# Optimization experiments

Hardware: AMD Instinct MI355X
Metric: run time of the kernel (lower is better)

The kernel has to match this reference:

```python
import jax, jax.numpy as jnp
import numpy as np

TSZ, BSZ, E, H = 1024, 8, 1024, 16


def setup_inputs() -> dict:
    key = jax.random.key(0)
    ks = jax.random.split(key, 7)
    s = 0.02
    return {
        "q": jax.random.normal(ks[0], (TSZ, BSZ, E), jnp.float32),
        "k": jax.random.normal(ks[1], (TSZ, BSZ, E), jnp.float32),
        "v": jax.random.normal(ks[2], (TSZ, BSZ, E), jnp.float32),
        "in_proj_weight": jax.random.normal(ks[3], (3 * E, E), jnp.float32) * s,
        "in_proj_bias": jax.random.normal(ks[4], (3 * E,), jnp.float32) * s,
        "out_proj_weight": jax.random.normal(ks[5], (E, E), jnp.float32) * s,
        "out_proj_bias": jax.random.normal(ks[6], (E,), jnp.float32) * s,
        "num_heads": H,
    }


def reference(q, k, v, in_proj_weight, in_proj_bias, out_proj_weight, out_proj_bias, num_heads):
    tsz, bsz, embed_dim = q.shape
    head_dim = embed_dim // num_heads
    scaling = float(head_dim) ** -0.5

    # in-projections (F.linear: x @ W.T + b), weight sliced into q/k/v chunks
    qp = q @ in_proj_weight[:embed_dim].T + in_proj_bias[:embed_dim]
    kp = k @ in_proj_weight[embed_dim:2 * embed_dim].T + in_proj_bias[embed_dim:2 * embed_dim]
    vp = v @ in_proj_weight[2 * embed_dim:].T + in_proj_bias[2 * embed_dim:]
    qp = qp * scaling

    # (tsz, bsz, E) -> (bsz*H, tsz, head_dim)
    def to_heads(x):
        return x.reshape(tsz, bsz * num_heads, head_dim).transpose(1, 0, 2)

    qh, kh, vh = to_heads(qp), to_heads(kp), to_heads(vp)

    # scaled dot-product attention (no mask, dropout p=0)
    scores = jnp.einsum('bqd,bkd->bqk', qh, kh)  # [bsz*H, tsz, tsz]
    weights = jax.nn.softmax(scores, axis=-1)
    attn = jnp.einsum('bqk,bkd->bqd', weights, vh)

    # back to (tsz, bsz, E), then out projection
    attn = attn.transpose(1, 0, 2).reshape(tsz, bsz, embed_dim)
    out = attn @ out_proj_weight.T + out_proj_bias
    return out
```

## Files before the change

### kernel.cpp

```cpp
#include <hip/hip_runtime.h>

typedef __bf16 bf16;
typedef __attribute__((ext_vector_type(8))) __bf16 v8bf;
typedef __attribute__((ext_vector_type(4))) __bf16 v4bf;
typedef __attribute__((ext_vector_type(4))) float f32x4;

static_assert(sizeof(v8bf) == 16, "v8bf must be 16B");

#define MFMA16(a, b, c) __builtin_amdgcn_mfma_f32_16x16x32_bf16((a), (b), (c), 0, 0, 0)

__device__ __forceinline__ void async_lds16(const bf16* g, bf16* l) {
  __builtin_amdgcn_global_load_lds(
      (__attribute__((address_space(1))) void*)(g),
      (__attribute__((address_space(3))) void*)(l), 16, 0, 0);
}

__global__ __launch_bounds__(256) void cvt_kernel(
    const float* __restrict__ q, const float* __restrict__ k,
    const float* __restrict__ v, const float* __restrict__ wi,
    const float* __restrict__ wo, bf16* __restrict__ xq, bf16* __restrict__ xk,
    bf16* __restrict__ xv, bf16* __restrict__ Wb, bf16* __restrict__ Wob) {
  int idx = blockIdx.x * 256 + threadIdx.x;
  const float4* src;
  v4bf* dst;
  int off;
  if (idx < 2097152)      { src = (const float4*)q;  dst = (v4bf*)xq;  off = idx; }
  else if (idx < 4194304) { src = (const float4*)k;  dst = (v4bf*)xk;  off = idx - 2097152; }
  else if (idx < 6291456) { src = (const float4*)v;  dst = (v4bf*)xv;  off = idx - 4194304; }
  else if (idx < 7077888) { src = (const float4*)wi; dst = (v4bf*)Wb;  off = idx - 6291456; }
  else                    { src = (const float4*)wo; dst = (v4bf*)Wob; off = idx - 7077888; }
  float4 f = src[off];
  v4bf b;
  b[0] = (bf16)f.x; b[1] = (bf16)f.y; b[2] = (bf16)f.z; b[3] = (bf16)f.w;
  dst[off] = b;
}

__global__ __launch_bounds__(256) void qkv_proj_kernel(
    const bf16* __restrict__ xq, const bf16* __restrict__ xk,
    const bf16* __restrict__ xv, const bf16* __restrict__ Wb,
    const float* __restrict__ bias, bf16* __restrict__ oq,
    bf16* __restrict__ ok, bf16* __restrict__ ov) {
  __shared__ bf16 Asm[128 * 64];
  __shared__ bf16 Bsm[128 * 64];
  const int L = blockIdx.x;
  const int rX = L & 7, rest = L >> 3;
  const int m0 = (rX * 8 + (rest & 7)) * 128;
  const int n0 = ((rest >> 3) & 7) * 128;
  const int c = rest >> 6;
  const bf16* X = (c == 0) ? xq : (c == 1) ? xk : xv;
  bf16* outp = (c == 0) ? oq : (c == 1) ? ok : ov;
  const int tid = threadIdx.x;
  const int w = tid >> 6, l = tid & 63, quad = l >> 4, lr = l & 15;
  const int wm = (w & 1) * 64, wn = (w >> 1) * 64;
  const bf16* Wbase = Wb + ((size_t)(c * 1024 + n0)) * 1024;

  int srow[4], skoff[4];
#pragma unroll
  for (int i = 0; i < 4; ++i) {
    const int chunk = i * 256 + tid;
    srow[i] = chunk >> 3;
    skoff[i] = ((chunk & 7) ^ (srow[i] & 7)) * 8;
  }
  int rslot[2];
#pragma unroll
  for (int h = 0; h < 2; ++h) rslot[h] = ((h * 4 + quad) ^ (lr & 7)) * 8;

  f32x4 acc[4][4] = {};
  for (int kt = 0; kt < 16; ++kt) {
    const int k0 = kt * 64;
#pragma unroll
    for (int i = 0; i < 4; ++i) {
      async_lds16(X + (size_t)(m0 + srow[i]) * 1024 + k0 + skoff[i],
                  &Asm[(i * 256 + (tid & ~63)) * 8]);
      async_lds16(Wbase + (size_t)srow[i] * 1024 + k0 + skoff[i],
                  &Bsm[(i * 256 + (tid & ~63)) * 8]);
    }
    __syncthreads();
    v8bf af[4][2], bfm[4][2];
#pragma unroll
    for (int rt = 0; rt < 4; ++rt)
#pragma unroll
      for (int h = 0; h < 2; ++h)
        af[rt][h] = *(const v8bf*)&Asm[(wm + rt * 16 + lr) * 64 + rslot[h]];
#pragma unroll
    for (int ct = 0; ct < 4; ++ct)
#pragma unroll
      for (int h = 0; h < 2; ++h)
        bfm[ct][h] = *(const v8bf*)&Bsm[(wn + ct * 16 + lr) * 64 + rslot[h]];
#pragma unroll
    for (int rt = 0; rt < 4; ++rt)
#pragma unroll
      for (int ct = 0; ct < 4; ++ct) {
        acc[rt][ct] = MFMA16(af[rt][0], bfm[ct][0], acc[rt][ct]);
        acc[rt][ct] = MFMA16(af[rt][1], bfm[ct][1], acc[rt][ct]);
      }
    __syncthreads();
  }

  const float scale = (c == 0) ? 0.125f : 1.0f;
#pragma unroll
  for (int rt = 0; rt < 4; ++rt) {
#pragma unroll
    for (int ct = 0; ct < 4; ++ct) {
      const int n = n0 + wn + ct * 16 + lr;
      const float bn = bias[c * 1024 + n];
      const int h = n >> 6, d = n & 63;
#pragma unroll
      for (int j = 0; j < 4; ++j) {
        const int m = m0 + wm + rt * 16 + quad * 4 + j;
        const int t = m >> 3, b = m & 7;
        const float val = (acc[rt][ct][j] + bn) * scale;
        outp[((size_t)((b * 16 + h) * 1024 + t)) * 64 + d] = (bf16)val;
      }
    }
  }
}

__global__ __launch_bounds__(256) void transpose_v_kernel(const bf16* __restrict__ vin,
                                                          bf16* __restrict__ vout) {
  __shared__ bf16 tile[64][72];
  const int bh = blockIdx.x;
  const int t0 = blockIdx.y * 64;
  const int tid = threadIdx.x;
  const int row = tid >> 2, cg = (tid & 3) * 16;
  const bf16* src = vin + ((size_t)bh * 1024 + t0 + row) * 64 + cg;
#pragma unroll
  for (int i = 0; i < 2; ++i) {
    v8bf x = *(const v8bf*)(src + i * 8);
#pragma unroll
    for (int jj = 0; jj < 8; ++jj) tile[row][cg + i * 8 + jj] = x[jj];
  }
  __syncthreads();
  const int d = tid >> 2, tg = (tid & 3) * 16;
  bf16* dst = vout + ((size_t)bh * 64 + d) * 1024 + t0 + tg;
  v8bf o0, o1;
#pragma unroll
  for (int i = 0; i < 8; ++i) o0[i] = tile[tg + i][d];
#pragma unroll
  for (int i = 0; i < 8; ++i) o1[i] = tile[tg + 8 + i][d];
  *(v8bf*)dst = o0;
  *(v8bf*)(dst + 8) = o1;
}

#define KSTR 72
#define VSTR 136

__global__ __launch_bounds__(256, 2) void attn_kernel(const bf16* __restrict__ qh,
                                                      const bf16* __restrict__ kh,
                                                      const bf16* __restrict__ vT,
                                                      bf16* __restrict__ attn_out) {
  __shared__ bf16 Ksm[128 * KSTR];
  __shared__ bf16 Vsm[64 * VSTR];
  __shared__ bf16 Psm[128 * VSTR];
  const int L = blockIdx.x;
  const int bh = (L & 7) * 16 + ((L >> 3) & 15);
  const int t0 = (L >> 7) * 128;
  const int tid = threadIdx.x;
  const int w = tid >> 6, l = tid & 63, quad = l >> 4, lr = l & 15;
  const int qr0 = t0 + w * 32;

  const bf16* khead = kh + (size_t)bh * 1024 * 64;
  const bf16* vhead = vT + (size_t)bh * 64 * 1024;

  const size_t qbase = ((size_t)bh * 1024 + qr0 + lr) * 64 + quad * 8;
  const v8bf bq00 = *(const v8bf*)(qh + qbase);
  const v8bf bq01 = *(const v8bf*)(qh + qbase + 32);
  const v8bf bq10 = *(const v8bf*)(qh + qbase + 1024);
  const v8bf bq11 = *(const v8bf*)(qh + qbase + 1024 + 32);

  const int krow = tid >> 1, kd = (tid & 1) * 32;
  const int vrow = tid >> 2, vk = (tid & 3) * 32;
  const bf16* kg = khead + (size_t)krow * 64 + kd;
  const bf16* vg = vhead + (size_t)vrow * 1024 + vk;
  bf16* Kw = &Ksm[krow * KSTR + kd];
  bf16* Vw = &Vsm[vrow * VSTR + vk];
  bf16* Pw = &Psm[w * 32 * VSTR];

  v8bf kst[4], vst[4];
#pragma unroll
  for (int i = 0; i < 4; ++i) kst[i] = *(const v8bf*)(kg + i * 8);
#pragma unroll
  for (int i = 0; i < 4; ++i) vst[i] = *(const v8bf*)(vg + i * 8);

  float rsum0 = 0.0f, rsum1 = 0.0f;
  f32x4 oacc0[4] = {}, oacc1[4] = {};

  for (int c = 0; c < 8; ++c) {
    __syncthreads();
#pragma unroll
    for (int i = 0; i < 4; ++i) *(v8bf*)(Kw + i * 8) = kst[i];
#pragma unroll
    for (int i = 0; i < 4; ++i) *(v8bf*)(Vw + i * 8) = vst[i];
    __syncthreads();
    if (c < 7) {
      const bf16* kg2 = kg + (size_t)(c + 1) * 128 * 64;
      const bf16* vg2 = vg + (c + 1) * 128;
#pragma unroll
      for (int i = 0; i < 4; ++i) kst[i] = *(const v8bf*)(kg2 + i * 8);
#pragma unroll
      for (int i = 0; i < 4; ++i) vst[i] = *(const v8bf*)(vg2 + i * 8);
    }

#pragma unroll
    for (int kt = 0; kt < 8; ++kt) {
      const v8bf ak0 = *(const v8bf*)&Ksm[(kt * 16 + lr) * KSTR + quad * 8];
      const v8bf ak1 = *(const v8bf*)&Ksm[(kt * 16 + lr) * KSTR + 32 + quad * 8];
      f32x4 a = {};
      a = MFMA16(ak0, bq00, a);
      a = MFMA16(ak1, bq01, a);
      f32x4 b = {};
      b = MFMA16(ak0, bq10, b);
      b = MFMA16(ak1, bq11, b);
      v4bf pb0, pb1;
#pragma unroll
      for (int j = 0; j < 4; ++j) {
        const float p0 = __expf(a[j]);
        const float p1 = __expf(b[j]);
        rsum0 += p0;
        rsum1 += p1;
        pb0[j] = (bf16)p0;
        pb1[j] = (bf16)p1;
      }
      *(v4bf*)(Pw + lr * VSTR + kt * 16 + quad * 4) = pb0;
      *(v4bf*)(Pw + (16 + lr) * VSTR + kt * 16 + quad * 4) = pb1;
    }

#pragma unroll
    for (int ks = 0; ks < 4; ++ks) {
      const v8bf pa0 = *(const v8bf*)(Pw + lr * VSTR + ks * 32 + quad * 8);
      const v8bf pa1 = *(const v8bf*)(Pw + (16 + lr) * VSTR + ks * 32 + quad * 8);
#pragma unroll
      for (int dt = 0; dt < 4; ++dt) {
        const v8bf vb = *(const v8bf*)&Vsm[(dt * 16 + lr) * VSTR + ks * 32 + quad * 8];
        oacc0[dt] = MFMA16(pa0, vb, oacc0[dt]);
        oacc1[dt] = MFMA16(pa1, vb, oacc1[dt]);
      }
    }
  }

  rsum0 += __shfl_xor(rsum0, 16);
  rsum0 += __shfl_xor(rsum0, 32);
  rsum1 += __shfl_xor(rsum1, 16);
  rsum1 += __shfl_xor(rsum1, 32);
  const float inv0 = 1.0f / rsum0;
  const float inv1 = 1.0f / rsum1;
  const int b = bh >> 4, h = bh & 15;
#pragma unroll
  for (int j = 0; j < 4; ++j) {
    const float i0 = __shfl(inv0, quad * 4 + j);
    const float i1 = __shfl(inv1, quad * 4 + j);
    const int t0j = qr0 + quad * 4 + j;
#pragma unroll
    for (int dt = 0; dt < 4; ++dt) {
      attn_out[((size_t)(t0j * 8 + b)) * 1024 + h * 64 + dt * 16 + lr] =
          (bf16)(oacc0[dt][j] * i0);
      attn_out[((size_t)((t0j + 16) * 8 + b)) * 1024 + h * 64 + dt * 16 + lr] =
          (bf16)(oacc1[dt][j] * i1);
    }
  }
}

__global__ __launch_bounds__(256) void out_proj_kernel(const bf16* __restrict__ A,
                                                       const bf16* __restrict__ Wob,
                                                       const float* __restrict__ bias,
                                                       float* __restrict__ out) {
  __shared__ bf16 Asm[128 * 64];
  __shared__ bf16 Bsm[128 * 64];
  const int L = blockIdx.x;
  const int m0 = ((L & 7) * 8 + ((L >> 3) & 7)) * 128;
  const int n0 = (L >> 6) * 128;
  const int tid = threadIdx.x;
  const int w = tid >> 6, l = tid & 63, quad = l >> 4, lr = l & 15;
  const int wm = (w & 1) * 64, wn = (w >> 1) * 64;

  int srow[4], skoff[4];
#pragma unroll
  for (int i = 0; i < 4; ++i) {
    const int chunk = i * 256 + tid;
    srow[i] = chunk >> 3;
    skoff[i] = ((chunk & 7) ^ (srow[i] & 7)) * 8;
  }
  int rslot[2];
#pragma unroll
  for (int h = 0; h < 2; ++h) rslot[h] = ((h * 4 + quad) ^ (lr & 7)) * 8;

  f32x4 acc[4][4] = {};
  for (int kt = 0; kt < 16; ++kt) {
    const int k0 = kt * 64;
#pragma unroll
    for (int i = 0; i < 4; ++i) {
      async_lds16(A + (size_t)(m0 + srow[i]) * 1024 + k0 + skoff[i],
                  &Asm[(i * 256 + (tid & ~63)) * 8]);
      async_lds16(Wob + (size_t)(n0 + srow[i]) * 1024 + k0 + skoff[i],
                  &Bsm[(i * 256 + (tid & ~63)) * 8]);
    }
    __syncthreads();
    v8bf af[4][2], bfm[4][2];
#pragma unroll
    for (int rt = 0; rt < 4; ++rt)
#pragma unroll
      for (int h = 0; h < 2; ++h)
        af[rt][h] = *(const v8bf*)&Asm[(wm + rt * 16 + lr) * 64 + rslot[h]];
#pragma unroll
    for (int ct = 0; ct < 4; ++ct)
#pragma unroll
      for (int h = 0; h < 2; ++h)
        bfm[ct][h] = *(const v8bf*)&Bsm[(wn + ct * 16 + lr) * 64 + rslot[h]];
#pragma unroll
    for (int rt = 0; rt < 4; ++rt)
#pragma unroll
      for (int ct = 0; ct < 4; ++ct) {
        acc[rt][ct] = MFMA16(af[rt][0], bfm[ct][0], acc[rt][ct]);
        acc[rt][ct] = MFMA16(af[rt][1], bfm[ct][1], acc[rt][ct]);
      }
    __syncthreads();
  }

#pragma unroll
  for (int rt = 0; rt < 4; ++rt)
#pragma unroll
    for (int ct = 0; ct < 4; ++ct) {
      const int n = n0 + wn + ct * 16 + lr;
      const float bn = bias[n];
#pragma unroll
      for (int j = 0; j < 4; ++j) {
        const int m = m0 + wm + rt * 16 + quad * 4 + j;
        out[(size_t)m * 1024 + n] = acc[rt][ct][j] + bn;
      }
    }
}

extern "C" void kernel_launch(void* const* d_in, const int* in_sizes, int n_in,
                              void* d_out, int out_size, void* d_ws, size_t ws_size,
                              hipStream_t stream) {
  const float* q  = (const float*)d_in[0];
  const float* k  = (const float*)d_in[1];
  const float* v  = (const float*)d_in[2];
  const float* wi = (const float*)d_in[3];
  const float* bi = (const float*)d_in[4];
  const float* wo = (const float*)d_in[5];
  const float* bo = (const float*)d_in[6];
  float* out = (float*)d_out;
  char* ws = (char*)d_ws;
  const size_t MB = (size_t)1 << 20;
  bf16* Wb     = (bf16*)(ws + 0 * MB);
  bf16* Wob    = (bf16*)(ws + 6 * MB);
  bf16* wsq    = (bf16*)(ws + 8 * MB);
  bf16* wsk    = (bf16*)(ws + 24 * MB);
  bf16* wsv    = (bf16*)(ws + 40 * MB);
  bf16* xv     = (bf16*)(ws + 56 * MB);
  bf16* wsvT   = (bf16*)(ws + 56 * MB);
  bf16* xq     = (bf16*)d_out;
  bf16* xk     = (bf16*)((char*)d_out + 16 * MB);
  bf16* wsattn = wsv;

  cvt_kernel<<<dim3(28672), dim3(256), 0, stream>>>(q, k, v, wi, wo, xq, xk, xv, Wb, Wob);
  qkv_proj_kernel<<<dim3(1536), dim3(256), 0, stream>>>(xq, xk, xv, Wb, bi, wsq, wsk, wsv);
  transpose_v_kernel<<<dim3(128, 16), dim3(256), 0, stream>>>(wsv, wsvT);
  attn_kernel<<<dim3(1024), dim3(256), 0, stream>>>(wsq, wsk, wsvT, wsattn);
  out_proj_kernel<<<dim3(512), dim3(256), 0, stream>>>(wsattn, Wob, bo, out);
}
```

Measured before the change: 302.4 us.

## Rewrite projection GEMMs as double-buffered 256x128 tiles with interleaved prefetch

Both projection GEMMs move to 512-thread blocks with 256x128 output tiles and double-buffered LDS. Each k-tile is split into four sub-phases that issue async global-to-LDS loads for the next tile while MFMAs run, using explicit vmcnt waits, raw barriers and setprio. This is meant to hide global load latency and the full __syncthreads stalls of the single-buffered loop. In exchange LDS use per block rises, launch bounds target 2 blocks per CU, and the hand-tuned waitcnt ordering is fragile.

Result: faster. 296.3 us (-2.0%).

```diff
diff --git a/kernel.cpp b/kernel.cpp
--- a/kernel.cpp
+++ b/kernel.cpp
@@ -35,85 +35,141 @@
   dst[off] = b;
 }
 
-__global__ __launch_bounds__(256) void qkv_proj_kernel(
+#define STAGE_A(S, MH, KO)                                                    \
+  do {                                                                        \
+    async_lds16(Xa + (size_t)((MH) * 128 + srA0) * 1024 + (KO) + skA0,        \
+                &Asm[S][MH][ldst]);                                           \
+    async_lds16(Xa + (size_t)((MH) * 128 + srA1) * 1024 + (KO) + skA1,        \
+                &Asm[S][MH][4096 + ldst]);                                    \
+  } while (0)
+
+#define STAGE_B(S, NH, KO)                                                    \
+  async_lds16(Wbase + (size_t)((NH) * 64 + srB) * 1024 + (KO) + skB,          \
+              &Bsm[S][NH][ldst])
+
+#define KTILE(S, NS, KN)                                                      \
+  do {                                                                        \
+    v8bf af0[4][2], af1[4][2], bf0[2], bf1[2];                                \
+                                                            \
+    _Pragma("unroll") for (int rt = 0; rt < 4; ++rt) {                        \
+      af0[rt][0] = *(const v8bf*)&Asm[S][0][aro + rt * 1024 + rslot0];        \
+      af0[rt][1] = *(const v8bf*)&Asm[S][0][aro + rt * 1024 + rslot1];        \
+    }                                                                         \
+    bf0[0] = *(const v8bf*)&Bsm[S][0][bro + rslot0];                          \
+    bf0[1] = *(const v8bf*)&Bsm[S][0][bro + rslot1];                          \
+    STAGE_A(NS, 0, KN);                                                       \
+    asm volatile("s_waitcnt vmcnt(2)" ::: "memory");                          \
+    __builtin_amdgcn_s_barrier();                                             \
+    __builtin_amdgcn_s_setprio(1);                                            \
+    _Pragma("unroll") for (int rt = 0; rt < 4; ++rt) {                        \
+      acc[rt][0] = MFMA16(af0[rt][0], bf0[0], acc[rt][0]);                    \
+      acc[rt][0] = MFMA16(af0[rt][1], bf0[1], acc[rt][0]);                    \
+    }                                                                         \
+    __builtin_amdgcn_s_setprio(0);                                            \
+                                                            \
+    _Pragma("unroll") for (int rt = 0; rt < 4; ++rt) {                        \
+      af1[rt][0] = *(const v8bf*)&Asm[S][1][aro + rt * 1024 + rslot0];        \
+      af1[rt][1] = *(const v8bf*)&Asm[S][1][aro + rt * 1024 + rslot1];        \
+    }                                                                         \
+    bf1[0] = *(const v8bf*)&Bsm[S][1][bro + rslot0];                          \
+    bf1[1] = *(const v8bf*)&Bsm[S][1][bro + rslot1];                          \
+    STAGE_B(NS, 0, KN);                                                       \
+    __builtin_amdgcn_s_barrier();                                             \
+    __builtin_amdgcn_s_setprio(1);                                            \
+    _Pragma("unroll") for (int rt = 0; rt < 4; ++rt) {                        \
+      acc[4 + rt][1] = MFMA16(af1[rt][0], bf1[0], acc[4 + rt][1]);            \
+      acc[4 + rt][1] = MFMA16(af1[rt][1], bf1[1], acc[4 + rt][1]);            \
+    }                                                                         \
+    __builtin_amdgcn_s_setprio(0);                                            \
+                                                            \
+    STAGE_A(NS, 1, KN);                                                       \
+    __builtin_amdgcn_s_barrier();                                             \
+    __builtin_amdgcn_s_setprio(1);                                            \
+    _Pragma("unroll") for (int rt = 0; rt < 4; ++rt) {                        \
+      acc[4 + rt][0] = MFMA16(af1[rt][0], bf0[0], acc[4 + rt][0]);            \
+      acc[4 + rt][0] = MFMA16(af1[rt][1], bf0[1], acc[4 + rt][0]);            \
+    }                                                                         \
+    __builtin_amdgcn_s_setprio(0);                                            \
+                                                            \
+    STAGE_B(NS, 1, KN);                                                       \
+    asm volatile("s_waitcnt vmcnt(3)" ::: "memory");                          \
+    __builtin_amdgcn_s_barrier();                                             \
+    __builtin_amdgcn_s_setprio(1);                                            \
+    _Pragma("unroll") for (int rt = 0; rt < 4; ++rt) {                        \
+      acc[rt][1] = MFMA16(af0[rt][0], bf1[0], acc[rt][1]);                    \
+      acc[rt][1] = MFMA16(af0[rt][1], bf1[1], acc[rt][1]);                    \
+    }                                                                         \
+    __builtin_amdgcn_s_setprio(0);                                            \
+  } while (0)
+
+#define GEMM_PRELUDE()                                                        \
+  const int tid = threadIdx.x;                                                \
+  const int w = tid >> 6, l = tid & 63, quad = l >> 4, lr = l & 15;           \
+  const int wmg = w >> 2, wng = w & 3;                                        \
+  const int srA0 = tid >> 3;                                                  \
+  const int skA0 = (((tid & 7) ^ (srA0 & 7)) * 8);                            \
+  const int srA1 = (512 + tid) >> 3;                                          \
+  const int skA1 = (((tid & 7) ^ (srA1 & 7)) * 8);                            \
+  const int srB = tid >> 3;                                                   \
+  const int skB = (((tid & 7) ^ (srB & 7)) * 8);                              \
+  const int ldst = (tid & ~63) * 8;                                           \
+  const int aro = (wmg * 64 + lr) * 64;                                       \
+  const int bro = (wng * 16 + lr) * 64;                                       \
+  const int rslot0 = ((quad) ^ (lr & 7)) * 8;                                 \
+  const int rslot1 = ((4 + quad) ^ (lr & 7)) * 8;                             \
+  f32x4 acc[8][2] = {};                                                       \
+        \
+  STAGE_A(0, 0, 0);                                                           \
+  STAGE_B(0, 0, 0);                                                           \
+  STAGE_A(0, 1, 0);                                                           \
+  STAGE_B(0, 1, 0);                                                           \
+  asm volatile("s_waitcnt vmcnt(3)" ::: "memory");                            \
+  __builtin_amdgcn_s_barrier();                                               \
+  _Pragma("unroll 1") for (int t = 0; t < 16; t += 2) {                       \
+    const int k1 = (t + 1) * 64;                                              \
+    const int k2 = (t == 14) ? 0 : (t + 2) * 64;  \
+    KTILE(0, 1, k1);                                                          \
+    KTILE(1, 0, k2);                                                          \
+  }                                                                           \
+  asm volatile("s_waitcnt vmcnt(0)" ::: "memory");
+
+__global__ __launch_bounds__(512, 2) void qkv_proj_kernel(
     const bf16* __restrict__ xq, const bf16* __restrict__ xk,
     const bf16* __restrict__ xv, const bf16* __restrict__ Wb,
     const float* __restrict__ bias, bf16* __restrict__ oq,
     bf16* __restrict__ ok, bf16* __restrict__ ov) {
-  __shared__ bf16 Asm[128 * 64];
-  __shared__ bf16 Bsm[128 * 64];
+  __shared__ bf16 Asm[2][2][128 * 64];
+  __shared__ bf16 Bsm[2][2][64 * 64];
   const int L = blockIdx.x;
-  const int rX = L & 7, rest = L >> 3;
-  const int m0 = (rX * 8 + (rest & 7)) * 128;
-  const int n0 = ((rest >> 3) & 7) * 128;
-  const int c = rest >> 6;
+  const int r = L & 7, rest = L >> 3;
+  const int m0 = (r * 4 + (rest & 3)) * 256;
+  const int n0 = ((rest >> 2) & 7) * 128;
+  const int c = rest >> 5;
   const bf16* X = (c == 0) ? xq : (c == 1) ? xk : xv;
   bf16* outp = (c == 0) ? oq : (c == 1) ? ok : ov;
-  const int tid = threadIdx.x;
-  const int w = tid >> 6, l = tid & 63, quad = l >> 4, lr = l & 15;
-  const int wm = (w & 1) * 64, wn = (w >> 1) * 64;
+  const bf16* Xa = X + (size_t)m0 * 1024;
   const bf16* Wbase = Wb + ((size_t)(c * 1024 + n0)) * 1024;
 
-  int srow[4], skoff[4];
-#pragma unroll
-  for (int i = 0; i < 4; ++i) {
-    const int chunk = i * 256 + tid;
-    srow[i] = chunk >> 3;
-    skoff[i] = ((chunk & 7) ^ (srow[i] & 7)) * 8;
-  }
-  int rslot[2];
-#pragma unroll
-  for (int h = 0; h < 2; ++h) rslot[h] = ((h * 4 + quad) ^ (lr & 7)) * 8;
-
-  f32x4 acc[4][4] = {};
-  for (int kt = 0; kt < 16; ++kt) {
-    const int k0 = kt * 64;
-#pragma unroll
-    for (int i = 0; i < 4; ++i) {
-      async_lds16(X + (size_t)(m0 + srow[i]) * 1024 + k0 + skoff[i],
-                  &Asm[(i * 256 + (tid & ~63)) * 8]);
-      async_lds16(Wbase + (size_t)srow[i] * 1024 + k0 + skoff[i],
-                  &Bsm[(i * 256 + (tid & ~63)) * 8]);
-    }
-    __syncthreads();
-    v8bf af[4][2], bfm[4][2];
+  GEMM_PRELUDE();
+
+  const float scale = (c == 0) ? 0.125f : 1.0f;
+#pragma unroll
+  for (int mh = 0; mh < 2; ++mh)
 #pragma unroll
     for (int rt = 0; rt < 4; ++rt)
 #pragma unroll
-      for (int h = 0; h < 2; ++h)
-        af[rt][h] = *(const v8bf*)&Asm[(wm + rt * 16 + lr) * 64 + rslot[h]];
-#pragma unroll
-    for (int ct = 0; ct < 4; ++ct)
-#pragma unroll
-      for (int h = 0; h < 2; ++h)
-        bfm[ct][h] = *(const v8bf*)&Bsm[(wn + ct * 16 + lr) * 64 + rslot[h]];
-#pragma unroll
-    for (int rt = 0; rt < 4; ++rt)
-#pragma unroll
-      for (int ct = 0; ct < 4; ++ct) {
-        acc[rt][ct] = MFMA16(af[rt][0], bfm[ct][0], acc[rt][ct]);
-        acc[rt][ct] = MFMA16(af[rt][1], bfm[ct][1], acc[rt][ct]);
+      for (int nh = 0; nh < 2; ++nh) {
+        const int n = n0 + nh * 64 + wng * 16 + lr;
+        const float bn = bias[c * 1024 + n];
+        const int hh = n >> 6, d = n & 63;
+#pragma unroll
+        for (int j = 0; j < 4; ++j) {
+          const int m = m0 + mh * 128 + wmg * 64 + rt * 16 + quad * 4 + j;
+          const int t_ = m >> 3, b = m & 7;
+          outp[((size_t)((b * 16 + hh) * 1024 + t_)) * 64 + d] =
+              (bf16)((acc[mh * 4 + rt][nh][j] + bn) * scale);
+        }
       }
-    __syncthreads();
-  }
-
-  const float scale = (c == 0) ? 0.125f : 1.0f;
-#pragma unroll
-  for (int rt = 0; rt < 4; ++rt) {
-#pragma unroll
-    for (int ct = 0; ct < 4; ++ct) {
-      const int n = n0 + wn + ct * 16 + lr;
-      const float bn = bias[c * 1024 + n];
-      const int h = n >> 6, d = n & 63;
-#pragma unroll
-      for (int j = 0; j < 4; ++j) {
-        const int m = m0 + wm + rt * 16 + quad * 4 + j;
-        const int t = m >> 3, b = m & 7;
-        const float val = (acc[rt][ct][j] + bn) * scale;
-        outp[((size_t)((b * 16 + h) * 1024 + t)) * 64 + d] = (bf16)val;
-      }
-    }
-  }
 }
 
 __global__ __launch_bounds__(256) void transpose_v_kernel(const bf16* __restrict__ vin,
@@ -260,74 +316,35 @@
   }
 }
 
-__global__ __launch_bounds__(256) void out_proj_kernel(const bf16* __restrict__ A,
-                                                       const bf16* __restrict__ Wob,
-                                                       const float* __restrict__ bias,
-                                                       float* __restrict__ out) {
-  __shared__ bf16 Asm[128 * 64];
-  __shared__ bf16 Bsm[128 * 64];
+__global__ __launch_bounds__(512, 2) void out_proj_kernel(const bf16* __restrict__ A,
+                                                          const bf16* __restrict__ Wob,
+                                                          const float* __restrict__ bias,
+                                                          float* __restrict__ out) {
+  __shared__ bf16 Asm[2][2][128 * 64];
+  __shared__ bf16 Bsm[2][2][64 * 64];
   const int L = blockIdx.x;
-  const int m0 = ((L & 7) * 8 + ((L >> 3) & 7)) * 128;
-  const int n0 = (L >> 6) * 128;
-  const int tid = threadIdx.x;
-  const int w = tid >> 6, l = tid & 63, quad = l >> 4, lr = l & 15;
-  const int wm = (w & 1) * 64, wn = (w >> 1) * 64;
-
-  int srow[4], skoff[4];
-#pragma unroll
-  for (int i = 0; i < 4; ++i) {
-    const int chunk = i * 256 + tid;
-    srow[i] = chunk >> 3;
-    skoff[i] = ((chunk & 7) ^ (srow[i] & 7)) * 8;
-  }
-  int rslot[2];
-#pragma unroll
-  for (int h = 0; h < 2; ++h) rslot[h] = ((h * 4 + quad) ^ (lr & 7)) * 8;
-
-  f32x4 acc[4][4] = {};
-  for (int kt = 0; kt < 16; ++kt) {
-    const int k0 = kt * 64;
-#pragma unroll
-    for (int i = 0; i < 4; ++i) {
-      async_lds16(A + (size_t)(m0 + srow[i]) * 1024 + k0 + skoff[i],
-                  &Asm[(i * 256 + (tid & ~63)) * 8]);
-      async_lds16(Wob + (size_t)(n0 + srow[i]) * 1024 + k0 + skoff[i],
-                  &Bsm[(i * 256 + (tid & ~63)) * 8]);
-    }
-    __syncthreads();
-    v8bf af[4][2], bfm[4][2];
+  const int r = L & 7, rest = L >> 3;
+  const int m0 = (r * 4 + (rest & 3)) * 256;
+  const int n0 = (rest >> 2) * 128;
+  const bf16* Xa = A + (size_t)m0 * 1024;
+  const bf16* Wbase = Wob + (size_t)n0 * 1024;
+
+  GEMM_PRELUDE();
+
+#pragma unroll
+  for (int mh = 0; mh < 2; ++mh)
 #pragma unroll
     for (int rt = 0; rt < 4; ++rt)
 #pragma unroll
-      for (int h = 0; h < 2; ++h)
-        af[rt][h] = *(const v8bf*)&Asm[(wm + rt * 16 + lr) * 64 + rslot[h]];
-#pragma unroll
-    for (int ct = 0; ct < 4; ++ct)
-#pragma unroll
-      for (int h = 0; h < 2; ++h)
-        bfm[ct][h] = *(const v8bf*)&Bsm[(wn + ct * 16 + lr) * 64 + rslot[h]];
-#pragma unroll
-    for (int rt = 0; rt < 4; ++rt)
-#pragma unroll
-      for (int ct = 0; ct < 4; ++ct) {
-        acc[rt][ct] = MFMA16(af[rt][0], bfm[ct][0], acc[rt][ct]);
-        acc[rt][ct] = MFMA16(af[rt][1], bfm[ct][1], acc[rt][ct]);
+      for (int nh = 0; nh < 2; ++nh) {
+        const int n = n0 + nh * 64 + wng * 16 + lr;
+        const float bn = bias[n];
+#pragma unroll
+        for (int j = 0; j < 4; ++j) {
+          const int m = m0 + mh * 128 + wmg * 64 + rt * 16 + quad * 4 + j;
+          out[(size_t)m * 1024 + n] = acc[mh * 4 + rt][nh][j] + bn;
+        }
       }
-    __syncthreads();
-  }
-
-#pragma unroll
-  for (int rt = 0; rt < 4; ++rt)
-#pragma unroll
-    for (int ct = 0; ct < 4; ++ct) {
-      const int n = n0 + wn + ct * 16 + lr;
-      const float bn = bias[n];
-#pragma unroll
-      for (int j = 0; j < 4; ++j) {
-        const int m = m0 + wm + rt * 16 + quad * 4 + j;
-        out[(size_t)m * 1024 + n] = acc[rt][ct][j] + bn;
-      }
-    }
 }
 
 extern "C" void kernel_launch(void* const* d_in, const int* in_sizes, int n_in,
@@ -355,8 +372,8 @@
   bf16* wsattn = wsv;
 
   cvt_kernel<<<dim3(28672), dim3(256), 0, stream>>>(q, k, v, wi, wo, xq, xk, xv, Wb, Wob);
-  qkv_proj_kernel<<<dim3(1536), dim3(256), 0, stream>>>(xq, xk, xv, Wb, bi, wsq, wsk, wsv);
+  qkv_proj_kernel<<<dim3(768), dim3(512), 0, stream>>>(xq, xk, xv, Wb, bi, wsq, wsk, wsv);
   transpose_v_kernel<<<dim3(128, 16), dim3(256), 0, stream>>>(wsv, wsvT);
   attn_kernel<<<dim3(1024), dim3(256), 0, stream>>>(wsq, wsk, wsvT, wsattn);
-  out_proj_kernel<<<dim3(512), dim3(256), 0, stream>>>(wsattn, Wob, bo, out);
-}
+  out_proj_kernel<<<dim3(512 / 2), dim3(512), 0, stream>>>(wsattn, Wob, bo, out);
+}
```
